# Kernel tuning notes

Measured on AMD Instinct MI355X. Metric: run time of the kernel, lower is better.

Reference implementation:

```python
import jax, jax.numpy as jnp
import numpy as np

B, N, FIN, FOUT, E = 2, 50000, 128, 64, 800000


def setup_inputs() -> dict:
    key = jax.random.key(0)
    ks = jax.random.split(key, 7)
    x = jax.random.normal(ks[0], (B, N, FIN), dtype=jnp.float32)
    W = jax.random.normal(ks[1], (FIN, FOUT), dtype=jnp.float32) * (1.0 / np.sqrt(FIN))
    W_self = jax.random.normal(ks[2], (FIN, FOUT), dtype=jnp.float32) * (1.0 / np.sqrt(FIN))
    b_self = jax.random.normal(ks[3], (FOUT,), dtype=jnp.float32) * 0.01
    edge_row = jax.random.randint(ks[4], (E,), 0, N, dtype=jnp.int32)
    edge_col = jax.random.randint(ks[5], (E,), 0, N, dtype=jnp.int32)
    edge_val = jax.random.uniform(ks[6], (E,), dtype=jnp.float32)
    return {"x": x, "W": W, "W_self": W_self, "b_self": b_self,
            "edge_row": edge_row, "edge_col": edge_col, "edge_val": edge_val}


def reference(x, W, W_self, b_self, edge_row, edge_col, edge_val):
    # x: (B, N, FIN); adjacency in COO form: out[r] += val * in[c]
    Bn, Nn, _ = x.shape
    Fo = W.shape[1]
    x_trans = jnp.einsum("bnf,fo->bno", x, W)               # (B, N, FOUT), no bias
    # Same layout trick as torch: sparse.mm over (N, B*FOUT)
    xr = x_trans.transpose(1, 0, 2).reshape(Nn, Bn * Fo)    # (N, B*FOUT)
    msgs = edge_val[:, None] * xr[edge_col]                  # (E, B*FOUT) gather
    agg = jax.ops.segment_sum(msgs, edge_row, num_segments=Nn)  # (N, B*FOUT) scatter-add
    agg = agg.reshape(Nn, Bn, Fo).transpose(1, 0, 2)         # (B, N, FOUT)
    self_c = jnp.einsum("bnf,fo->bno", x, W_self) + b_self   # Linear with bias
    return jax.nn.relu(self_c + agg)
```

## Files before the change

### kernel.cpp

```cpp
#include <hip/hip_runtime.h>
#include <hip/hip_fp16.h>

#define Bc   2
#define Nn   50000
#define FINc 128
#define FOUTc 64
#define Mtot (Bc * Nn)
#define CCOMB 128
#define GB 1563
#define SB 1563
#define CAP 64
#define ZTOT (Nn * 16)

typedef __bf16 bf16x8 __attribute__((ext_vector_type(8)));
typedef float  f32x4  __attribute__((ext_vector_type(4)));

static __device__ inline unsigned short f2bf(float f) {
    unsigned int u = __float_as_uint(f);
    u += 0x7fffu + ((u >> 16) & 1u);
    return (unsigned short)(u >> 16);
}

__global__ __launch_bounds__(256) void prep(
    const float* __restrict__ W, const float* __restrict__ Ws,
    unsigned short* __restrict__ Bp, int* __restrict__ zbase)
{
    if (blockIdx.x < 8) {
        const int idx = blockIdx.x * 256 + threadIdx.x;
        const int lane = idx & 63;
        const int kt   = (idx >> 6) & 3;
        const int nt   = idx >> 8;
        const int n    = nt * 16 + (lane & 15);
        const int k0   = kt * 32 + (lane >> 4) * 8;
        unsigned short o8[8];
#pragma unroll
        for (int j = 0; j < 8; ++j) {
            const int f = k0 + j;
            const float v = (n < 64) ? W[f * FOUTc + n] : Ws[f * FOUTc + (n - 64)];
            o8[j] = f2bf(v);
        }
        *(uint4*)&Bp[(size_t)idx * 8] = *(uint4*)o8;
    } else {
        const int i4 = (blockIdx.x - 8) * 1024 + threadIdx.x * 4;
        if (i4 + 4 <= ZTOT)
            *(int4*)&zbase[i4] = make_int4(0, 0, 0, 0);
    }
}

__global__ __launch_bounds__(256) void scatter_gemm(
    const float* __restrict__ x, const unsigned short* __restrict__ Bp,
    const float* __restrict__ bself,
    unsigned short* __restrict__ xrb, float* __restrict__ outp,
    const int* __restrict__ erow, const int* __restrict__ ecol,
    const float* __restrict__ evalv, int* __restrict__ cntp,
    unsigned int* __restrict__ cvp, int E)
{
    const int b = blockIdx.x;

    if (!(b & 1)) {
        const int sb = b >> 1;
        const int e0 = sb * 512 + threadIdx.x;
        const int e1 = e0 + 256;
        if (e0 < E) {
            const int   r = erow[e0];
            const int   c = ecol[e0];
            const float v = evalv[e0];
            const int k = atomicAdd(&cntp[(size_t)r * 16], 1);
            if (k < CAP)
                cvp[((size_t)r << 6) + k] =
                    ((unsigned int)__half_as_ushort(__float2half(v)) << 17) | (unsigned int)c;
        }
        if (e1 < E) {
            const int   r = erow[e1];
            const int   c = ecol[e1];
            const float v = evalv[e1];
            const int k = atomicAdd(&cntp[(size_t)r * 16], 1);
            if (k < CAP)
                cvp[((size_t)r << 6) + k] =
                    ((unsigned int)__half_as_ushort(__float2half(v)) << 17) | (unsigned int)c;
        }
        return;
    }

    const int gb   = b >> 1;
    const int lane = threadIdx.x & 63;
    const int quad = lane >> 4;
    const int mbase = gb * 64 + (threadIdx.x >> 6) * 16;

    const int mrow   = mbase + (lane & 15);
    const int mclamp = (mrow < Mtot) ? mrow : (Mtot - 1);
    const float* __restrict__ xrow = &x[(size_t)mclamp * FINc + quad * 8];

    float4 xv[8];
#pragma unroll
    for (int kt = 0; kt < 4; ++kt) {
        xv[2 * kt]     = *(const float4*)&xrow[kt * 32];
        xv[2 * kt + 1] = *(const float4*)&xrow[kt * 32 + 4];
    }

    f32x4 acc[8] = {};

#pragma unroll
    for (int kt = 0; kt < 4; ++kt) {
        const float4 xa = xv[2 * kt];
        const float4 xb = xv[2 * kt + 1];
        bf16x8 bf;
        bf[0] = (__bf16)xa.x; bf[1] = (__bf16)xa.y;
        bf[2] = (__bf16)xa.z; bf[3] = (__bf16)xa.w;
        bf[4] = (__bf16)xb.x; bf[5] = (__bf16)xb.y;
        bf[6] = (__bf16)xb.z; bf[7] = (__bf16)xb.w;

        const bf16x8* __restrict__ abase =
            (const bf16x8*)&Bp[(size_t)(kt * 64 + lane) * 8];
#pragma unroll
        for (int nt = 0; nt < 8; ++nt) {
            const bf16x8 af = abase[nt * 4 * 64];
            acc[nt] = __builtin_amdgcn_mfma_f32_16x16x32_bf16(af, bf, acc[nt], 0, 0, 0);
        }
    }

    const int m = mbase + (lane & 15);
    if (m < Mtot) {
        const int bb = (m >= Nn) ? 1 : 0;
        const int n = m - bb * Nn;
        unsigned short* __restrict__ xp = &xrb[(size_t)n * CCOMB + bb * FOUTc];
        const int cq = quad * 4;
#pragma unroll
        for (int nt = 0; nt < 4; ++nt) {
            const int c = nt * 16 + cq;
            unsigned short h[4];
            h[0] = f2bf(acc[nt][0]); h[1] = f2bf(acc[nt][1]);
            h[2] = f2bf(acc[nt][2]); h[3] = f2bf(acc[nt][3]);
            *(uint2*)&xp[c] = *(uint2*)h;
        }
        float* __restrict__ op = &outp[(size_t)m * FOUTc];
#pragma unroll
        for (int nt = 4; nt < 8; ++nt) {
            const int o = (nt - 4) * 16 + cq;
            const float4 b4 = *(const float4*)&bself[o];
            float4 v;
            v.x = acc[nt][0] + b4.x; v.y = acc[nt][1] + b4.y;
            v.z = acc[nt][2] + b4.z; v.w = acc[nt][3] + b4.w;
            *(float4*)&op[o] = v;
        }
    }
}

#define GATHP(W, PRED, ACC)                                                   \
    {                                                                         \
        const unsigned int w = (W);                                           \
        unsigned int col = w & 0x1FFFFu;                                      \
        col = (col < Nn) ? col : 0u;           \
        const float vv = (PRED) ? __half2float(__ushort_as_half(              \
                             (unsigned short)(w >> 17))) : 0.0f;              \
        const uint4 raw = *(const uint4*)&xrb[(size_t)col * CCOMB + c0];      \
        ACC[0] = fmaf(vv, __uint_as_float(raw.x << 16),         ACC[0]);      \
        ACC[1] = fmaf(vv, __uint_as_float(raw.x & 0xffff0000u), ACC[1]);      \
        ACC[2] = fmaf(vv, __uint_as_float(raw.y << 16),         ACC[2]);      \
        ACC[3] = fmaf(vv, __uint_as_float(raw.y & 0xffff0000u), ACC[3]);      \
        ACC[4] = fmaf(vv, __uint_as_float(raw.z << 16),         ACC[4]);      \
        ACC[5] = fmaf(vv, __uint_as_float(raw.z & 0xffff0000u), ACC[5]);      \
        ACC[6] = fmaf(vv, __uint_as_float(raw.w << 16),         ACC[6]);      \
        ACC[7] = fmaf(vv, __uint_as_float(raw.w & 0xffff0000u), ACC[7]);      \
    }

__global__ __launch_bounds__(256) void row_gather(
    const int* __restrict__ cntp, const unsigned int* __restrict__ cvp,
    const unsigned short* __restrict__ xrb, float* __restrict__ outp)
{
    const int j    = blockIdx.x;
    const int low3 = j & 7;
    const int h    = (low3 >= 4) ? 1 : 0;
    const int ord  = (j >> 3) * 4 + (low3 & 3);
    int n = ord * 4 + (threadIdx.x >> 6);
    n = __builtin_amdgcn_readfirstlane(n);

    const int lane = threadIdx.x & 63;
    const int slot = lane >> 3;
    const int c0   = h * 64 + (lane & 7) * 8;
    const unsigned int* __restrict__ seg = &cvp[(size_t)n << 6];

    const int kc = min(cntp[(size_t)n * 16], CAP);
    const unsigned int u0 = seg[slot];
    const unsigned int u1 = seg[8 + slot];

    float aA[8] = {0.f, 0.f, 0.f, 0.f, 0.f, 0.f, 0.f, 0.f};

    GATHP(u0, slot < kc,     aA);
    GATHP(u1, slot + 8 < kc, aA);

    for (int e = 16 + slot; e < kc; e += 8) {
        const unsigned int u = seg[e];
        GATHP(u, true, aA);
    }

#pragma unroll
    for (int i = 0; i < 8; ++i) {
        aA[i] += __shfl_down(aA[i], 8);
        aA[i] += __shfl_down(aA[i], 16);
        aA[i] += __shfl_down(aA[i], 32);
    }

    if (lane < 8) {
        const size_t m = (size_t)h * Nn + n;
        const int o = lane * 8;
        float* __restrict__ op = &outp[m * FOUTc + o];
        float4 s0 = *(float4*)&op[0];
        float4 s1 = *(float4*)&op[4];
        s0.x = fmaxf(s0.x + aA[0], 0.0f); s0.y = fmaxf(s0.y + aA[1], 0.0f);
        s0.z = fmaxf(s0.z + aA[2], 0.0f); s0.w = fmaxf(s0.w + aA[3], 0.0f);
        s1.x = fmaxf(s1.x + aA[4], 0.0f); s1.y = fmaxf(s1.y + aA[5], 0.0f);
        s1.z = fmaxf(s1.z + aA[6], 0.0f); s1.w = fmaxf(s1.w + aA[7], 0.0f);
        *(float4*)&op[0] = s0;
        *(float4*)&op[4] = s1;
    }
}

extern "C" void kernel_launch(void* const* d_in, const int* in_sizes, int n_in,
                              void* d_out, int out_size, void* d_ws, size_t ws_size,
                              hipStream_t stream)
{
    const float* x    = (const float*)d_in[0];
    const float* W    = (const float*)d_in[1];
    const float* Ws   = (const float*)d_in[2];
    const float* bs   = (const float*)d_in[3];
    const int*   erow = (const int*)d_in[4];
    const int*   ecol = (const int*)d_in[5];
    const float* eval = (const float*)d_in[6];
    float* outp = (float*)d_out;
    const int E = in_sizes[4];

    unsigned short* xrb = (unsigned short*)d_ws;
    unsigned int*   cvp = (unsigned int*)(xrb + (size_t)Nn * CCOMB);
    int*            cntp = (int*)(cvp + ((size_t)Nn << 6));
    unsigned short* Bp  = (unsigned short*)(cntp + (size_t)Nn * 16);

    prep<<<8 + (ZTOT + 1023) / 1024, 256, 0, stream>>>(W, Ws, Bp, cntp);

    scatter_gemm<<<SB + GB, 256, 0, stream>>>(x, Bp, bs, xrb, outp,
                                              erow, ecol, eval, cntp, cvp, E);

    row_gather<<<Nn / 2, 256, 0, stream>>>(cntp, cvp, xrb, outp);
}
```

Baseline: 199.0 us.

## Replace global-atomic edge scatter with two-pass bucketed binning through LDS

Global per-row atomic scatter of edges into CSR-like lists is replaced by a two-phase binning. Phase one histograms edges per block into 128-row buckets, reserves slots with one global atomic per bucket, and writes coalesced staged records. Phase two builds per-row lists in shared memory and writes them out densely with counts. The GEMM is split into its own kernel and the large count-zeroing pass is dropped. This trades scattered global atomics for extra passes and kernel launches, and adds a per-bucket capacity cap that could drop edges on skewed inputs.

```diff
diff --git a/kernel.cpp b/kernel.cpp
--- a/kernel.cpp
+++ b/kernel.cpp
@@ -8,9 +8,13 @@
 #define Mtot (Bc * Nn)
 #define CCOMB 128
 #define GB 1563
-#define SB 1563
 #define CAP 64
-#define ZTOT (Nn * 16)
+
+#define NRNG   128
+#define NBUCK  391
+#define ABLK   256
+#define RECCAP 3200
+#define BCAP   2432
 
 typedef __bf16 bf16x8 __attribute__((ext_vector_type(8)));
 typedef float  f32x4  __attribute__((ext_vector_type(4)));
@@ -23,7 +27,7 @@
 
 __global__ __launch_bounds__(256) void prep(
     const float* __restrict__ W, const float* __restrict__ Ws,
-    unsigned short* __restrict__ Bp, int* __restrict__ zbase)
+    unsigned short* __restrict__ Bp, unsigned int* __restrict__ bfill)
 {
     if (blockIdx.x < 8) {
         const int idx = blockIdx.x * 256 + threadIdx.x;
@@ -41,48 +45,16 @@
         }
         *(uint4*)&Bp[(size_t)idx * 8] = *(uint4*)o8;
     } else {
-        const int i4 = (blockIdx.x - 8) * 1024 + threadIdx.x * 4;
-        if (i4 + 4 <= ZTOT)
-            *(int4*)&zbase[i4] = make_int4(0, 0, 0, 0);
-    }
-}
-
-__global__ __launch_bounds__(256) void scatter_gemm(
+        for (int i = threadIdx.x; i < NBUCK; i += 256) bfill[i] = 0u;
+    }
+}
+
+__global__ __launch_bounds__(256) void gemm(
     const float* __restrict__ x, const unsigned short* __restrict__ Bp,
     const float* __restrict__ bself,
-    unsigned short* __restrict__ xrb, float* __restrict__ outp,
-    const int* __restrict__ erow, const int* __restrict__ ecol,
-    const float* __restrict__ evalv, int* __restrict__ cntp,
-    unsigned int* __restrict__ cvp, int E)
-{
-    const int b = blockIdx.x;
-
-    if (!(b & 1)) {
-        const int sb = b >> 1;
-        const int e0 = sb * 512 + threadIdx.x;
-        const int e1 = e0 + 256;
-        if (e0 < E) {
-            const int   r = erow[e0];
-            const int   c = ecol[e0];
-            const float v = evalv[e0];
-            const int k = atomicAdd(&cntp[(size_t)r * 16], 1);
-            if (k < CAP)
-                cvp[((size_t)r << 6) + k] =
-                    ((unsigned int)__half_as_ushort(__float2half(v)) << 17) | (unsigned int)c;
-        }
-        if (e1 < E) {
-            const int   r = erow[e1];
-            const int   c = ecol[e1];
-            const float v = evalv[e1];
-            const int k = atomicAdd(&cntp[(size_t)r * 16], 1);
-            if (k < CAP)
-                cvp[((size_t)r << 6) + k] =
-                    ((unsigned int)__half_as_ushort(__float2half(v)) << 17) | (unsigned int)c;
-        }
-        return;
-    }
-
-    const int gb   = b >> 1;
+    unsigned short* __restrict__ xrb, float* __restrict__ outp)
+{
+    const int gb   = blockIdx.x;
     const int lane = threadIdx.x & 63;
     const int quad = lane >> 4;
     const int mbase = gb * 64 + (threadIdx.x >> 6) * 16;
@@ -143,6 +115,108 @@
             v.z = acc[nt][2] + b4.z; v.w = acc[nt][3] + b4.w;
             *(float4*)&op[o] = v;
         }
+    }
+}
+
+__global__ __launch_bounds__(256) void bin_a(
+    const int* __restrict__ erow, const int* __restrict__ ecol,
+    const float* __restrict__ evalv, unsigned int* __restrict__ bfill,
+    uint2* __restrict__ stage, int E, int ec)
+{
+    __shared__ unsigned int hist[512];
+    __shared__ unsigned int incl[512];
+    __shared__ unsigned int gbase[NBUCK];
+    __shared__ unsigned int cur[NBUCK];
+    __shared__ unsigned int recs[RECCAP * 2];
+
+    const int tid = threadIdx.x;
+    const int e0 = blockIdx.x * ec;
+    int e1 = e0 + ec; if (e1 > E) e1 = E;
+    if (e1 - e0 > RECCAP) e1 = e0 + RECCAP;
+    const int tot = e1 - e0;
+
+    hist[tid] = 0u; hist[tid + 256] = 0u;
+    __syncthreads();
+
+    for (int e = e0 + tid; e < e1; e += 256) {
+        const int r = erow[e];
+        atomicAdd(&hist[r >> 7], 1u);
+    }
+    __syncthreads();
+
+    incl[tid] = hist[tid]; incl[tid + 256] = hist[tid + 256];
+    __syncthreads();
+    for (int off = 1; off < 512; off <<= 1) {
+        const unsigned int a0 = (tid >= off) ? incl[tid - off] : 0u;
+        const unsigned int a1 = ((tid + 256) >= off) ? incl[tid + 256 - off] : 0u;
+        __syncthreads();
+        incl[tid] += a0; incl[tid + 256] += a1;
+        __syncthreads();
+    }
+
+    for (int i = tid; i < NBUCK; i += 256) {
+        const unsigned int c = hist[i];
+        cur[i]   = incl[i] - c;
+        gbase[i] = c ? atomicAdd(&bfill[i], c) : 0u;
+    }
+    __syncthreads();
+
+    for (int e = e0 + tid; e < e1; e += 256) {
+        const int   r = erow[e];
+        const int   c = ecol[e];
+        const float v = evalv[e];
+        const int  nb = r >> 7;
+        const unsigned int k = atomicAdd(&cur[nb], 1u);
+        recs[2 * k]     = ((unsigned int)__half_as_ushort(__float2half(v)) << 17) |
+                          (unsigned int)c;
+        recs[2 * k + 1] = ((unsigned int)nb << 7) | (unsigned int)(r & 127);
+    }
+    __syncthreads();
+
+    for (int j = tid; j < tot; j += 256) {
+        const unsigned int vc   = recs[2 * j];
+        const unsigned int meta = recs[2 * j + 1];
+        const int nb = (int)(meta >> 7);
+        const unsigned int excl = incl[nb] - hist[nb];
+        const unsigned int slot = gbase[nb] + ((unsigned int)j - excl);
+        if (slot < BCAP)
+            stage[(size_t)nb * BCAP + slot] = make_uint2(vc, meta);
+    }
+}
+
+__global__ __launch_bounds__(256) void bin_b(
+    const unsigned int* __restrict__ bfill, const uint2* __restrict__ stage,
+    unsigned int* __restrict__ cvp, int* __restrict__ cntp)
+{
+    __shared__ unsigned int lists[NRNG * CAP];
+    __shared__ unsigned int lcnt[NRNG];
+
+    const int tid = threadIdx.x;
+    const int nb  = blockIdx.x;
+    const int row0 = nb << 7;
+    int nrows = Nn - row0; if (nrows > NRNG) nrows = NRNG;
+
+    for (int i = tid; i < NRNG; i += 256) lcnt[i] = 0u;
+    __syncthreads();
+
+    unsigned int cnt = bfill[nb];
+    if (cnt > BCAP) cnt = BCAP;
+    const uint2* __restrict__ seg = &stage[(size_t)nb * BCAP];
+
+    for (unsigned int j = tid; j < cnt; j += 256) {
+        const uint2 rec = seg[j];
+        const int rl = (int)(rec.y & 127u);
+        const unsigned int k = atomicAdd(&lcnt[rl], 1u);
+        if (k < CAP) lists[(rl << 6) + k] = rec.x;
+    }
+    __syncthreads();
+
+    unsigned int* __restrict__ dst = &cvp[(size_t)row0 << 6];
+    const int words = nrows << 6;
+    for (int i = tid; i < words; i += 256) dst[i] = lists[i];
+    for (int rl = tid; rl < nrows; rl += 256) {
+        const unsigned int c = lcnt[rl];
+        cntp[(size_t)(row0 + rl) * 16] = (int)(c < CAP ? c : CAP);
     }
 }
 
@@ -234,11 +308,17 @@
     unsigned int*   cvp = (unsigned int*)(xrb + (size_t)Nn * CCOMB);
     int*            cntp = (int*)(cvp + ((size_t)Nn << 6));
     unsigned short* Bp  = (unsigned short*)(cntp + (size_t)Nn * 16);
-
-    prep<<<8 + (ZTOT + 1023) / 1024, 256, 0, stream>>>(W, Ws, Bp, cntp);
-
-    scatter_gemm<<<SB + GB, 256, 0, stream>>>(x, Bp, bs, xrb, outp,
-                                              erow, ecol, eval, cntp, cvp, E);
+    unsigned int*   bfill = (unsigned int*)(Bp + 16384);
+    uint2*          stage = (uint2*)(bfill + 512);
+
+    const int ec = (E + ABLK - 1) / ABLK;
+
+    prep<<<9, 256, 0, stream>>>(W, Ws, Bp, bfill);
+
+    gemm<<<GB, 256, 0, stream>>>(x, Bp, bs, xrb, outp);
+
+    bin_a<<<ABLK, 256, 0, stream>>>(erow, ecol, eval, bfill, stage, E, ec);
+    bin_b<<<NBUCK, 256, 0, stream>>>(bfill, stage, cvp, cntp);
 
     row_gather<<<Nn / 2, 256, 0, stream>>>(cntp, cvp, xrb, outp);
 }
```

New measurement: 185.3 us. 6.9% less time.
